# Kernel tuning notes

Hardware: AMD Instinct MI355X
Metric: run time of the kernel (lower is better)

Reference implementation:

```python
import jax, jax.numpy as jnp
import numpy as np

N_NODES = 100000
N_EDGES = 3200000
D_IN = 256
D_OUT = 256


def setup_inputs() -> dict:
    key = jax.random.key(0)
    k1, k2, k3, k4, k5, k6 = jax.random.split(key, 6)
    x = jax.random.normal(k1, (N_NODES, D_IN), dtype=jnp.float32)
    edge_src = jax.random.randint(k2, (N_EDGES,), 0, N_NODES, dtype=jnp.int32)
    edge_dst = jax.random.randint(k3, (N_EDGES,), 0, N_NODES, dtype=jnp.int32)
    edge_weight = jax.random.uniform(k4, (N_EDGES,), dtype=jnp.float32)
    weight = jax.random.normal(k5, (D_IN, D_OUT), dtype=jnp.float32) * 0.02
    bias = jax.random.uniform(k6, (D_OUT,), dtype=jnp.float32)
    return {"x": x, "edge_src": edge_src, "edge_dst": edge_dst,
            "edge_weight": edge_weight, "weight": weight, "bias": bias}


def reference(x, edge_src, edge_dst, edge_weight, weight, bias):
    # support = X @ W  (dense GEMM)
    support = x @ weight  # [N, D_OUT]
    # output = A @ support, A given as COO edges (dst <- src with weight)
    msgs = support[edge_src] * edge_weight[:, None]  # [E, D_OUT]
    out = jax.ops.segment_sum(msgs, edge_dst, num_segments=N_NODES)  # [N, D_OUT]
    return out + bias
```

## Files before the change

### kernel.cpp

```cpp
#include <hip/hip_runtime.h>
#include <hip/hip_bf16.h>

#define N_NODES 100000
#define N_EDGES 3200000
#define DDIM    256
#define M_PAD   100096
#define NBKT    782
#define BCAP    4608
#define EPB     2048
#define NB_BINA 1563
#define NB_GEMM 1564
#define GCAP    2432

typedef __attribute__((ext_vector_type(8))) short short8;
typedef __attribute__((ext_vector_type(4))) float f32x4;

typedef const __attribute__((address_space(1))) void gvoid_t;
typedef __attribute__((address_space(3))) void lvoid_t;

__device__ __forceinline__ void load_lds16(const void* g, void* l) {
  __builtin_amdgcn_global_load_lds((gvoid_t*)g, (lvoid_t*)l, 16, 0, 0);
}

__device__ __forceinline__ unsigned short f2bf(float f) {
  __hip_bfloat16 h = __float2bfloat16(f);
  return *(unsigned short*)&h;
}
__device__ __forceinline__ float bflo(unsigned u) { return __uint_as_float(u << 16); }
__device__ __forceinline__ float bfhi(unsigned u) { return __uint_as_float(u & 0xffff0000u); }

__global__ void convw_kernel(const float* __restrict__ w, unsigned short* __restrict__ wt,
                             int* __restrict__ gcur) {
  int t = blockIdx.x * blockDim.x + threadIdx.x;
  int n = t >> 8, k = t & 255;
  wt[t] = f2bf(w[k * 256 + n]);
  if (t < NBKT) gcur[t] = 0;
}

__global__ __launch_bounds__(256) void gemm_binA_kernel(
    const float* __restrict__ x, const unsigned short* __restrict__ wt,
    unsigned short* __restrict__ sup,
    const int* __restrict__ src, const int* __restrict__ dst,
    const float* __restrict__ wgt,
    int* __restrict__ gcur, unsigned long long* __restrict__ region) {
  __shared__ __align__(16) char smem[34816];
  const int bid = blockIdx.x;
  const int t = threadIdx.x;

  if (bid >= NB_BINA) {
    unsigned short* As = (unsigned short*)smem;
    unsigned short* Bs = (unsigned short*)(smem + 8192);
    const int g  = bid - NB_BINA;
    const int m0 = (g >> 1) * 128;
    const int n0 = (g & 1) * 128;
    const int w    = t >> 6;
    const int lane = t & 63;
    const int quad = lane >> 4;
    const int l15  = lane & 15;
    const int wr   = w >> 1, wc = w & 1;
    const int srow   = lane >> 2;
    const int schunk = (lane & 3) * 8;

    f32x4 acc[4][4] = {};

    for (int kt = 0; kt < 256; kt += 32) {
#pragma unroll
      for (int j = 0; j < 4; ++j) {
        int f = j * 256 + t;
        int row = f >> 3, c4 = (f & 7) * 4;
        int xr = m0 + row; if (xr >= N_NODES) xr = N_NODES - 1;
        float4 v = *(const float4*)(x + (size_t)xr * 256 + kt + c4);
        ushort4 o;
        o.x = f2bf(v.x); o.y = f2bf(v.y); o.z = f2bf(v.z); o.w = f2bf(v.w);
        *(ushort4*)(As + row * 32 + c4) = o;
      }
#pragma unroll
      for (int i = 0; i < 2; ++i) {
        int r = w * 32 + i * 16 + srow;
        load_lds16(wt + ((size_t)(n0 + r) * 256 + kt + schunk),
                   Bs + (w * 32 + i * 16) * 32);
      }
      __syncthreads();

      short8 a[4], b[4];
#pragma unroll
      for (int mi = 0; mi < 4; ++mi)
        a[mi] = *(const short8*)(As + (wr * 64 + mi * 16 + l15) * 32 + quad * 8);
#pragma unroll
      for (int ni = 0; ni < 4; ++ni)
        b[ni] = *(const short8*)(Bs + (wc * 64 + ni * 16 + l15) * 32 + quad * 8);

#pragma unroll
      for (int mi = 0; mi < 4; ++mi)
#pragma unroll
        for (int ni = 0; ni < 4; ++ni)
          acc[mi][ni] = __builtin_amdgcn_mfma_f32_16x16x32_bf16(a[mi], b[ni], acc[mi][ni], 0, 0, 0);
      __syncthreads();
    }

#pragma unroll
    for (int mi = 0; mi < 4; ++mi) {
#pragma unroll
      for (int r = 0; r < 4; ++r) {
        size_t row = (size_t)(m0 + wr * 64 + mi * 16 + quad * 4 + r);
#pragma unroll
        for (int ni = 0; ni < 4; ++ni) {
          int col = n0 + wc * 64 + ni * 16 + l15;
          sup[row * 256 + col] = f2bf(acc[mi][ni][r]);
        }
      }
    }
    return;
  }

  unsigned long long* staged = (unsigned long long*)smem;
  unsigned short* sbkt = (unsigned short*)(smem + 16384);
  int* lhist  = (int*)(smem + 20480);
  int* lstart = (int*)(smem + 23608);
  int* lcur   = (int*)(smem + 26736);
  int* gb     = (int*)(smem + 29864);
  int* csum   = (int*)(smem + 32992);

  const int e0 = bid * EPB;
  const int ecnt = min(EPB, N_EDGES - e0);

  for (int i = t; i < NBKT; i += 256) lhist[i] = 0;
  __syncthreads();
  for (int k = t; k < ecnt; k += 256)
    atomicAdd(&lhist[dst[e0 + k] >> 7], 1);
  __syncthreads();

  int i0 = 4 * t;
  int a0 = (i0 + 0 < NBKT) ? lhist[i0 + 0] : 0;
  int a1 = (i0 + 1 < NBKT) ? lhist[i0 + 1] : 0;
  int a2 = (i0 + 2 < NBKT) ? lhist[i0 + 2] : 0;
  int a3 = (i0 + 3 < NBKT) ? lhist[i0 + 3] : 0;
  int s = a0 + a1 + a2 + a3;
  csum[t] = s;
  __syncthreads();
  for (int off = 1; off < 256; off <<= 1) {
    int v = (t >= off) ? csum[t - off] : 0;
    __syncthreads();
    csum[t] += v;
    __syncthreads();
  }
  int base = csum[t] - s;
  if (i0 + 0 < NBKT) lstart[i0 + 0] = base; base += a0;
  if (i0 + 1 < NBKT) lstart[i0 + 1] = base; base += a1;
  if (i0 + 2 < NBKT) lstart[i0 + 2] = base; base += a2;
  if (i0 + 3 < NBKT) lstart[i0 + 3] = base;
  __syncthreads();

  for (int i = t; i < NBKT; i += 256) {
    int c = lhist[i];
    int off = c ? atomicAdd(&gcur[i], c) : 0;
    gb[i] = i * BCAP + off;
    lcur[i] = lstart[i];
  }
  __syncthreads();

  for (int k = t; k < ecnt; k += 256) {
    int d  = dst[e0 + k];
    int sr = src[e0 + k];
    float wv = wgt[e0 + k];
    int b = d >> 7;
    int p = atomicAdd(&lcur[b], 1);
    staged[p] = ((unsigned long long)__float_as_uint(wv) << 32) |
                ((unsigned)(d & 127) << 17) | (unsigned)sr;
    sbkt[p] = (unsigned short)b;
  }
  __syncthreads();

  for (int j = t; j < ecnt; j += 256) {
    int b = sbkt[j];
    int addr = gb[b] + (j - lstart[b]);
    if (addr < (b + 1) * BCAP) region[addr] = staged[j];
  }
}

__global__ __launch_bounds__(256) void csr_gather_kernel(
    const unsigned long long* __restrict__ region,
    const int* __restrict__ gcur,
    const unsigned short* __restrict__ sup,
    const float* __restrict__ bias,
    float* __restrict__ out) {
  __shared__ unsigned long long lcsr[GCAP];
  __shared__ int lhist[64], loff[64], lcur[64];
  const int t = threadIdx.x;
  const int b = blockIdx.x;
  const int h = blockIdx.y;
  const int cnt = min(gcur[b], BCAP);
  const int base = b * BCAP;

  if (t < 64) lhist[t] = 0;
  __syncthreads();
  for (int j = t; j < cnt; j += 256) {
    unsigned lo = (unsigned)(region[base + j] & 0xffffffffu);
    int dl = (int)((lo >> 17) & 127);
    if ((dl >> 6) == h) atomicAdd(&lhist[dl & 63], 1);
  }
  __syncthreads();
  if (t < 64) loff[t] = lhist[t];
  __syncthreads();
  for (int off = 1; off < 64; off <<= 1) {
    int v = (t >= off && t < 64) ? loff[t - off] : 0;
    __syncthreads();
    if (t < 64) loff[t] += v;
    __syncthreads();
  }
  if (t < 64) { loff[t] -= lhist[t]; lcur[t] = loff[t]; }
  __syncthreads();
  for (int j = t; j < cnt; j += 256) {
    unsigned long long e = region[base + j];
    int dl = (int)((e >> 17) & 127);
    if ((dl >> 6) == h) {
      int p = atomicAdd(&lcur[dl & 63], 1);
      if (p < GCAP) lcsr[p] = e;
    }
  }
  __syncthreads();

  const int wv = t >> 6;
  const int c0 = (t & 63) * 4;
  float4 bv = *(const float4*)(bias + c0);

  for (int dl = wv; dl < 64; dl += 4) {
    int node = b * 128 + h * 64 + dl;
    if (node >= N_NODES) continue;
    int start = loff[dl];
    int end   = min(lcur[dl], GCAP);
    float a0 = bv.x, a1 = bv.y, a2 = bv.z, a3 = bv.w;

    int i = start;
    for (; i + 2 <= end; i += 2) {
      unsigned long long m0 = lcsr[i];
      unsigned long long m1 = lcsr[i + 1];
      int   s0 = (int)(m0 & 0x1ffffu);
      float w0 = __uint_as_float((unsigned)(m0 >> 32));
      int   s1 = (int)(m1 & 0x1ffffu);
      float w1 = __uint_as_float((unsigned)(m1 >> 32));
      uint2 p0 = *(const uint2*)(sup + (size_t)s0 * 256 + c0);
      uint2 p1 = *(const uint2*)(sup + (size_t)s1 * 256 + c0);
      a0 = fmaf(w0, bflo(p0.x), a0);
      a1 = fmaf(w0, bfhi(p0.x), a1);
      a2 = fmaf(w0, bflo(p0.y), a2);
      a3 = fmaf(w0, bfhi(p0.y), a3);
      a0 = fmaf(w1, bflo(p1.x), a0);
      a1 = fmaf(w1, bfhi(p1.x), a1);
      a2 = fmaf(w1, bflo(p1.y), a2);
      a3 = fmaf(w1, bfhi(p1.y), a3);
    }
    if (i < end) {
      unsigned long long m0 = lcsr[i];
      int   s0 = (int)(m0 & 0x1ffffu);
      float w0 = __uint_as_float((unsigned)(m0 >> 32));
      uint2 p0 = *(const uint2*)(sup + (size_t)s0 * 256 + c0);
      a0 = fmaf(w0, bflo(p0.x), a0);
      a1 = fmaf(w0, bfhi(p0.x), a1);
      a2 = fmaf(w0, bflo(p0.y), a2);
      a3 = fmaf(w0, bfhi(p0.y), a3);
    }
    *(float4*)(out + (size_t)node * 256 + c0) = make_float4(a0, a1, a2, a3);
  }
}

extern "C" void kernel_launch(void* const* d_in, const int* in_sizes, int n_in,
                              void* d_out, int out_size, void* d_ws, size_t ws_size,
                              hipStream_t stream) {
  const float* x        = (const float*)d_in[0];
  const int*   edge_src = (const int*)d_in[1];
  const int*   edge_dst = (const int*)d_in[2];
  const float* edge_w   = (const float*)d_in[3];
  const float* weight   = (const float*)d_in[4];
  const float* bias     = (const float*)d_in[5];
  float* out = (float*)d_out;

  char* ws = (char*)d_ws;
  size_t off = 0;
  auto alloc = [&](size_t bytes) -> void* {
    void* p = ws + off;
    off = (off + bytes + 255) & ~(size_t)255;
    return p;
  };

  unsigned short* wt  = (unsigned short*)alloc(256 * 256 * 2);
  unsigned short* sup = (unsigned short*)alloc((size_t)M_PAD * 256 * 2);
  unsigned long long* region = (unsigned long long*)alloc((size_t)NBKT * BCAP * 8);
  int* gcur = (int*)alloc(NBKT * 4);

  convw_kernel<<<256, 256, 0, stream>>>(weight, wt, gcur);
  gemm_binA_kernel<<<NB_BINA + NB_GEMM, 256, 0, stream>>>(x, wt, sup,
                                                          edge_src, edge_dst, edge_w,
                                                          gcur, region);
  csr_gather_kernel<<<dim3(NBKT, 2), 256, 0, stream>>>(region, gcur, sup, bias, out);
}
```

Baseline: 504.1 us.

## Double-buffer GEMM LDS tiles and double edges per binning block

```diff
diff --git a/kernel.cpp b/kernel.cpp
--- a/kernel.cpp
+++ b/kernel.cpp
@@ -7,10 +7,11 @@
 #define M_PAD   100096
 #define NBKT    782
 #define BCAP    4608
-#define EPB     2048
-#define NB_BINA 1563
+#define EPB     4096
+#define NB_BINA 782
 #define NB_GEMM 1564
 #define GCAP    2432
+#define SMEM_BYTES 50432
 
 typedef __attribute__((ext_vector_type(8))) short short8;
 typedef __attribute__((ext_vector_type(4))) float f32x4;
@@ -37,19 +38,21 @@
   if (t < NBKT) gcur[t] = 0;
 }
 
-__global__ __launch_bounds__(256) void gemm_binA_kernel(
+__global__ __launch_bounds__(256, 3) void gemm_binA_kernel(
     const float* __restrict__ x, const unsigned short* __restrict__ wt,
     unsigned short* __restrict__ sup,
     const int* __restrict__ src, const int* __restrict__ dst,
     const float* __restrict__ wgt,
     int* __restrict__ gcur, unsigned long long* __restrict__ region) {
-  __shared__ __align__(16) char smem[34816];
+  __shared__ __align__(16) char smem[SMEM_BYTES];
   const int bid = blockIdx.x;
   const int t = threadIdx.x;
 
   if (bid >= NB_BINA) {
-    unsigned short* As = (unsigned short*)smem;
-    unsigned short* Bs = (unsigned short*)(smem + 8192);
+    unsigned short* As0 = (unsigned short*)smem;
+    unsigned short* Bs0 = (unsigned short*)(smem + 8192);
+    unsigned short* As1 = (unsigned short*)(smem + 16384);
+    unsigned short* Bs1 = (unsigned short*)(smem + 24576);
     const int g  = bid - NB_BINA;
     const int m0 = (g >> 1) * 128;
     const int n0 = (g & 1) * 128;
@@ -63,38 +66,72 @@
 
     f32x4 acc[4][4] = {};
 
-    for (int kt = 0; kt < 256; kt += 32) {
-#pragma unroll
-      for (int j = 0; j < 4; ++j) {
-        int f = j * 256 + t;
-        int row = f >> 3, c4 = (f & 7) * 4;
-        int xr = m0 + row; if (xr >= N_NODES) xr = N_NODES - 1;
-        float4 v = *(const float4*)(x + (size_t)xr * 256 + kt + c4);
-        ushort4 o;
-        o.x = f2bf(v.x); o.y = f2bf(v.y); o.z = f2bf(v.z); o.w = f2bf(v.w);
-        *(ushort4*)(As + row * 32 + c4) = o;
-      }
-#pragma unroll
-      for (int i = 0; i < 2; ++i) {
-        int r = w * 32 + i * 16 + srow;
-        load_lds16(wt + ((size_t)(n0 + r) * 256 + kt + schunk),
-                   Bs + (w * 32 + i * 16) * 32);
+#define A_LOAD(kt, va)                                                        \
+    do { _Pragma("unroll")                                                    \
+      for (int j = 0; j < 4; ++j) {                                           \
+        int row = j * 32 + (t >> 3);                                          \
+        int xr = m0 + row; if (xr >= N_NODES) xr = N_NODES - 1;               \
+        va[j] = *(const float4*)(x + (size_t)xr * 256 + (kt) + (t & 7) * 4);  \
+      } } while (0)
+#define A_STORE(va, asb)                                                      \
+    do { _Pragma("unroll")                                                    \
+      for (int j = 0; j < 4; ++j) {                                           \
+        int row = j * 32 + (t >> 3);                                          \
+        ushort4 o;                                                            \
+        o.x = f2bf(va[j].x); o.y = f2bf(va[j].y);                             \
+        o.z = f2bf(va[j].z); o.w = f2bf(va[j].w);                             \
+        *(ushort4*)((asb) + row * 32 + (t & 7) * 4) = o;                      \
+      } } while (0)
+#define B_LOAD(kt, bsb)                                                       \
+    do { _Pragma("unroll")                                                    \
+      for (int i = 0; i < 2; ++i) {                                           \
+        int r = w * 32 + i * 16 + srow;                                       \
+        load_lds16(wt + ((size_t)(n0 + r) * 256 + (kt) + schunk),             \
+                   (bsb) + (w * 32 + i * 16) * 32);                           \
+      } } while (0)
+#define COMPUTE(asb, bsb)                                                     \
+    do {                                                                      \
+      short8 a[4], b[4];                                                      \
+      _Pragma("unroll")                                                       \
+      for (int mi = 0; mi < 4; ++mi)                                          \
+        a[mi] = *(const short8*)((asb) + (wr * 64 + mi * 16 + l15) * 32 + quad * 8); \
+      _Pragma("unroll")                                                       \
+      for (int ni = 0; ni < 4; ++ni)                                          \
+        b[ni] = *(const short8*)((bsb) + (wc * 64 + ni * 16 + l15) * 32 + quad * 8); \
+      _Pragma("unroll")                                                       \
+      for (int mi = 0; mi < 4; ++mi)                                          \
+        _Pragma("unroll")                                                     \
+        for (int ni = 0; ni < 4; ++ni)                                        \
+          acc[mi][ni] = __builtin_amdgcn_mfma_f32_16x16x32_bf16(a[mi], b[ni], acc[mi][ni], 0, 0, 0); \
+    } while (0)
+
+    {
+      float4 va[4];
+      A_LOAD(0, va);
+      A_STORE(va, As0);
+      B_LOAD(0, Bs0);
+    }
+    __syncthreads();
+    for (int kp = 0; kp < 4; ++kp) {
+      const int kt1 = kp * 64 + 32;
+      {
+        float4 va[4];
+        A_LOAD(kt1, va);
+        COMPUTE(As0, Bs0);
+        A_STORE(va, As1);
+        B_LOAD(kt1, Bs1);
       }
       __syncthreads();
-
-      short8 a[4], b[4];
-#pragma unroll
-      for (int mi = 0; mi < 4; ++mi)
-        a[mi] = *(const short8*)(As + (wr * 64 + mi * 16 + l15) * 32 + quad * 8);
-#pragma unroll
-      for (int ni = 0; ni < 4; ++ni)
-        b[ni] = *(const short8*)(Bs + (wc * 64 + ni * 16 + l15) * 32 + quad * 8);
-
-#pragma unroll
-      for (int mi = 0; mi < 4; ++mi)
-#pragma unroll
-        for (int ni = 0; ni < 4; ++ni)
-          acc[mi][ni] = __builtin_amdgcn_mfma_f32_16x16x32_bf16(a[mi], b[ni], acc[mi][ni], 0, 0, 0);
+      if (kp < 3) {
+        const int kt2 = kp * 64 + 64;
+        float4 vb[4];
+        A_LOAD(kt2, vb);
+        COMPUTE(As1, Bs1);
+        A_STORE(vb, As0);
+        B_LOAD(kt2, Bs0);
+      } else {
+        COMPUTE(As1, Bs1);
+      }
       __syncthreads();
     }
 
@@ -114,12 +151,12 @@
   }
 
   unsigned long long* staged = (unsigned long long*)smem;
-  unsigned short* sbkt = (unsigned short*)(smem + 16384);
-  int* lhist  = (int*)(smem + 20480);
-  int* lstart = (int*)(smem + 23608);
-  int* lcur   = (int*)(smem + 26736);
-  int* gb     = (int*)(smem + 29864);
-  int* csum   = (int*)(smem + 32992);
+  unsigned short* sbkt = (unsigned short*)(smem + 32768);
+  int* lstart = (int*)(smem + 40960);
+  int* lcur   = (int*)(smem + 44088);
+  int* gb     = (int*)(smem + 47216);
+  int* lhist  = (int*)smem;
+  int* csum   = (int*)(smem + 3200);
 
   const int e0 = bid * EPB;
   const int ecnt = min(EPB, N_EDGES - e0);
```

Result: no change. 495.1 us (-1.8%).
